# Performance work log

Hardware: AMD Instinct MI355X
Metric: run time of the kernel (lower is better)

The kernel has to match this reference:

```python
import jax, jax.numpy as jnp
import numpy as np

N_EMBD = 1024
N_HEAD = 16
B, L = 4, 2048


def setup_inputs() -> dict:
    key = jax.random.key(0)
    ks = jax.random.split(key, 5)
    scale = 1.0 / np.sqrt(N_EMBD)
    x = jax.random.normal(ks[0], (B, L, N_EMBD), dtype=jnp.float32)
    # nn.Linear(n_embd, n_embd, bias=False) weights, stored torch-style (out, in)
    Wq = jax.random.uniform(ks[1], (N_EMBD, N_EMBD), jnp.float32, -scale, scale)
    Wk = jax.random.uniform(ks[2], (N_EMBD, N_EMBD), jnp.float32, -scale, scale)
    Wv = jax.random.uniform(ks[3], (N_EMBD, N_EMBD), jnp.float32, -scale, scale)
    Wp = jax.random.uniform(ks[4], (N_EMBD, N_EMBD), jnp.float32, -scale, scale)
    attn_mask = jnp.ones((B, L), dtype=jnp.int32)
    return {"x": x, "Wq": Wq, "Wk": Wk, "Wv": Wv, "Wp": Wp, "attn_mask": attn_mask}


def reference(x, Wq, Wk, Wv, Wp, attn_mask):
    Bq, Lq, C = x.shape
    hd = C // N_HEAD
    # torch Linear: y = x @ W.T
    def split_heads(y):
        return y.reshape(Bq, Lq, N_HEAD, hd).transpose(0, 2, 1, 3)  # (B,H,L,hd)
    q = split_heads(x @ Wq.T)
    k = split_heads(x @ Wk.T)
    v = split_heads(x @ Wv.T)
    att = jnp.einsum("bhqd,bhkd->bhqk", q, k) / np.sqrt(hd)  # (B,H,L,L)
    causal = jnp.tril(jnp.ones((Lq, Lq), dtype=bool))
    neg_inf = jnp.float32(-jnp.inf)
    att = jnp.where(causal[None, None, :, :], att, neg_inf)
    pad = (attn_mask != 0)[:, None, None, :]  # (B,1,1,L) key-side padding mask
    att = jnp.where(pad, att, neg_inf)
    att = jax.nn.softmax(att, axis=-1)
    y = jnp.einsum("bhqk,bhkd->bhqd", att, v)
    y = y.transpose(0, 2, 1, 3).reshape(Bq, Lq, C)
    return y @ Wp.T
```

## Files before the change

### kernel.cpp

```cpp
#include <hip/hip_runtime.h>

typedef __attribute__((ext_vector_type(8))) short short8;
typedef __attribute__((ext_vector_type(4))) float floatx4;

#define CEMB 1024
#define NHEAD 16
#define HD 64
#define BATCH 4
#define SEQ 2048

#define BARRIER() asm volatile("s_waitcnt lgkmcnt(0)\n\ts_barrier" ::: "memory")

__device__ __forceinline__ unsigned short f2bf(float f) {
    union { float f; unsigned int i; } x; x.f = f;
    unsigned int r = x.i + 0x7FFFu + ((x.i >> 16) & 1u);
    return (unsigned short)(r >> 16);
}
__device__ __forceinline__ unsigned int packbf_trunc(float a, float b) {
    union { float f; unsigned int u; } x, y; x.f = a; y.f = b;
    return (x.u >> 16) | (y.u & 0xFFFF0000u);
}

#define GLD16(gp, lp) \
    __builtin_amdgcn_global_load_lds((const __attribute__((address_space(1))) void*)(gp), \
                                     (__attribute__((address_space(3))) void*)(lp), 16, 0, 0)

__global__ void cast_x(const float* __restrict__ src, unsigned short* __restrict__ dst, int n4) {
    int i = blockIdx.x * blockDim.x + threadIdx.x;
    if (i < n4) {
        float4 v = ((const float4*)src)[i];
        ushort4 o;
        o.x = f2bf(v.x); o.y = f2bf(v.y); o.z = f2bf(v.z); o.w = f2bf(v.w);
        ((ushort4*)dst)[i] = o;
    }
}

__global__ void cast_w(const float* __restrict__ w0, const float* __restrict__ w1,
                       const float* __restrict__ w2, const float* __restrict__ w3,
                       unsigned short* __restrict__ o0, unsigned short* __restrict__ o1,
                       unsigned short* __restrict__ o2, unsigned short* __restrict__ o3) {
    int which = blockIdx.y;
    const float* src = which == 0 ? w0 : which == 1 ? w1 : which == 2 ? w2 : w3;
    unsigned short* dst = which == 0 ? o0 : which == 1 ? o1 : which == 2 ? o2 : o3;
    float scale = (which == 0) ? 0.125f * 1.44269504088896f : 1.0f;
    int i = blockIdx.x * blockDim.x + threadIdx.x;
    float4 v = ((const float4*)src)[i];
    ushort4 o;
    o.x = f2bf(v.x * scale); o.y = f2bf(v.y * scale);
    o.z = f2bf(v.z * scale); o.w = f2bf(v.w * scale);
    ((ushort4*)dst)[i] = o;
}


#define MFMA __builtin_amdgcn_mfma_f32_16x16x32_bf16

#define PH(Ab, Bb, mh, nh) do {                                                 \
    short8 af[4][2], bfr[2][2];                                                 \
    _Pragma("unroll")                                                           \
    for (int mm = 0; mm < 4; ++mm) {                                            \
        af[mm][0] = *(const short8*)((Ab) + aOffR + (mh)*4096 + mm*1024 + ck0); \
        af[mm][1] = *(const short8*)((Ab) + aOffR + (mh)*4096 + mm*1024 + ck1); \
    }                                                                           \
    _Pragma("unroll")                                                           \
    for (int nn = 0; nn < 2; ++nn) {                                            \
        bfr[nn][0] = *(const short8*)((Bb) + bOffR + (nh)*2048 + nn*1024 + ck0);\
        bfr[nn][1] = *(const short8*)((Bb) + bOffR + (nh)*2048 + nn*1024 + ck1);\
    }                                                                           \
    __builtin_amdgcn_s_setprio(1);                                              \
    _Pragma("unroll")                                                           \
    for (int mm = 0; mm < 4; ++mm)                                              \
        _Pragma("unroll")                                                       \
        for (int nn = 0; nn < 2; ++nn) {                                        \
            acc[(mh)*4+mm][(nh)*2+nn] = MFMA(af[mm][0], bfr[nn][0],             \
                                             acc[(mh)*4+mm][(nh)*2+nn], 0,0,0); \
            acc[(mh)*4+mm][(nh)*2+nn] = MFMA(af[mm][1], bfr[nn][1],             \
                                             acc[(mh)*4+mm][(nh)*2+nn], 0,0,0); \
        }                                                                       \
    __builtin_amdgcn_s_setprio(0);                                              \
    __builtin_amdgcn_sched_barrier(0);                                          \
} while (0)

#define STAGE(Ab, Bb, k0) do {                                                  \
    GLD16(aS + (k0),             (Ab) + aLA);                                   \
    GLD16(aS + (k0) +  8 * CEMB, (Ab) + aLA + 512);                             \
    if constexpr (MH == 2) {                                                    \
        GLD16(aS + (k0) + 16 * CEMB, (Ab) + aLA + 1024);                        \
        GLD16(aS + (k0) + 24 * CEMB, (Ab) + aLA + 1536);                        \
    }                                                                           \
    GLD16(bS + (k0),             (Bb) + aLB);                                   \
    GLD16(bS + (k0) +  8 * CEMB, (Bb) + aLB + 512);                             \
    GLD16(bS + (k0) + 16 * CEMB, (Bb) + aLB + 1024);                            \
    GLD16(bS + (k0) + 24 * CEMB, (Bb) + aLB + 1536);                            \
} while (0)

#define PH4(Ab, Bb, MHL, t, do_stage) do {                                      \
    short8 af[4][2], bfr[2][2];                                                 \
    _Pragma("unroll")                                                           \
    for (int mm = 0; mm < 4; ++mm) {                                            \
        af[mm][0] = *(const short8*)((Ab) + aOffR + (MHL)*4096 + mm*1024 + ck0);\
        af[mm][1] = *(const short8*)((Ab) + aOffR + (MHL)*4096 + mm*1024 + ck1);\
    }                                                                           \
    _Pragma("unroll")                                                           \
    for (int nn = 0; nn < 2; ++nn) {                                            \
        bfr[nn][0] = *(const short8*)((Bb) + bOffR + 2048 + nn*1024 + ck0);     \
        bfr[nn][1] = *(const short8*)((Bb) + bOffR + 2048 + nn*1024 + ck1);     \
    }                                                                           \
    asm volatile("s_waitcnt lgkmcnt(0)\n\ts_barrier" ::: "memory");             \
    __builtin_amdgcn_sched_barrier(0);                                          \
    if (do_stage) STAGE(Ab, Bb, ((t) + 2) * 64);                                \
    __builtin_amdgcn_s_setprio(1);                                              \
    _Pragma("unroll")                                                           \
    for (int mm = 0; mm < 4; ++mm)                                              \
        _Pragma("unroll")                                                       \
        for (int nn = 0; nn < 2; ++nn) {                                        \
            acc[(MHL)*4+mm][2+nn] = MFMA(af[mm][0], bfr[nn][0],                 \
                                         acc[(MHL)*4+mm][2+nn], 0,0,0);         \
            acc[(MHL)*4+mm][2+nn] = MFMA(af[mm][1], bfr[nn][1],                 \
                                         acc[(MHL)*4+mm][2+nn], 0,0,0);         \
        }                                                                       \
    __builtin_amdgcn_s_setprio(0);                                              \
    __builtin_amdgcn_sched_barrier(0);                                          \
} while (0)

#define TILE(t, drain, do_stage) do {                                           \
    unsigned short* Ab = &As[(t) & 1][0];                                       \
    unsigned short* Bb = &Bs[(t) & 1][0];                                       \
    if (drain) { asm volatile("s_waitcnt vmcnt(0)" ::: "memory"); }             \
    else if constexpr (MH == 2) { asm volatile("s_waitcnt vmcnt(8)" ::: "memory"); } \
    else { asm volatile("s_waitcnt vmcnt(6)" ::: "memory"); }                   \
    asm volatile("s_barrier" ::: "memory");                                     \
    if constexpr (MH == 2) {                                                    \
        PH(Ab, Bb, 0, 0); PH(Ab, Bb, 1, 0); PH(Ab, Bb, 0, 1);                   \
        PH4(Ab, Bb, 1, t, do_stage);                                            \
    } else {                                                                    \
        PH(Ab, Bb, 0, 0);                                                       \
        PH4(Ab, Bb, 0, t, do_stage);                                            \
    }                                                                           \
} while (0)

template<int MH>
__launch_bounds__(512, 2)
__global__ void gemm_t(const unsigned short* __restrict__ A,
                       const unsigned short* __restrict__ W,
                       void* __restrict__ O0, void* __restrict__ O1,
                       void* __restrict__ O2, int mode, int ntn) {
    __shared__ unsigned short As[2][MH * 8192];
    __shared__ unsigned short Bs[2][16384];

    int nwg = gridDim.x;
    int bid = blockIdx.x;
    int wg = (bid & 7) * (nwg >> 3) + (bid >> 3);
    int mt = wg / ntn;
    int nt = wg - mt * ntn;
    int m0 = mt * (MH * 128), n0 = nt * 256;

    int tid = threadIdx.x;
    int wave = tid >> 6, lane = tid & 63;
    int l16 = lane & 15, quad = lane >> 4;
    int wm = wave >> 2, wn = wave & 3;

    int srow = lane >> 3;
    int scol = ((lane & 7) ^ srow) * 8;
    const unsigned short* aS = A + (size_t)(m0 + wave * (MH * 16) + srow) * CEMB + scol;
    const unsigned short* bS = W + (size_t)(n0 + wave * 32 + srow) * CEMB + scol;
    int aLA = wave * (MH * 1024);
    int aLB = wave * 2048;

    int aOffR = (wm * (MH * 64) + l16) * 64;
    int bOffR = (wn * 64 + l16) * 64;
    int ck0 = (quad ^ (l16 & 7)) * 8;
    int ck1 = ck0 ^ 32;

    floatx4 acc[MH * 4][4];
    #pragma unroll
    for (int mm = 0; mm < MH * 4; ++mm)
        #pragma unroll
        for (int nn = 0; nn < 4; ++nn) acc[mm][nn] = (floatx4){0.f, 0.f, 0.f, 0.f};

    STAGE(&As[0][0], &Bs[0][0], 0);
    STAGE(&As[1][0], &Bs[1][0], 64);

    #pragma unroll 2
    for (int t = 0; t < 14; ++t) { TILE(t, false, true); }
    TILE(14, false, false);
    TILE(15, true, false);

    if (mode == 1) {
        float* Of = (float*)O0;
        #pragma unroll
        for (int mf = 0; mf < MH * 4; ++mf)
            #pragma unroll
            for (int j = 0; j < 4; ++j) {
                int m = m0 + wm * (MH * 64) + mf * 16 + quad * 4 + j;
                #pragma unroll
                for (int nf = 0; nf < 4; ++nf) {
                    int n = n0 + wn * 64 + nf * 16 + l16;
                    Of[(size_t)m * CEMB + n] = acc[mf][nf][j];
                }
            }
    } else {
        int which = n0 >> 10;
        unsigned short* out = (unsigned short*)(which == 0 ? O0 : which == 1 ? O1 : O2);
        if (which < 2) {
            #pragma unroll
            for (int mf = 0; mf < MH * 4; ++mf)
                #pragma unroll
                for (int j = 0; j < 4; ++j) {
                    int m = m0 + wm * (MH * 64) + mf * 16 + quad * 4 + j;
                    int bb = m >> 11, ll = m & (SEQ - 1);
                    #pragma unroll
                    for (int nf = 0; nf < 4; ++nf) {
                        int n = (n0 & (CEMB - 1)) + wn * 64 + nf * 16 + l16;
                        int h = n >> 6, d = n & (HD - 1);
                        out[(size_t)((bb * NHEAD + h) * SEQ + ll) * HD + d] =
                            f2bf(acc[mf][nf][j]);
                    }
                }
        } else {
            #pragma unroll
            for (int mf = 0; mf < MH * 4; ++mf) {
                int m = m0 + wm * (MH * 64) + mf * 16 + quad * 4;
                int bb = m >> 11, ll = m & (SEQ - 1);
                #pragma unroll
                for (int nf = 0; nf < 4; ++nf) {
                    int n = (n0 & (CEMB - 1)) + wn * 64 + nf * 16 + l16;
                    int h = n >> 6, d = n & (HD - 1);
                    ushort4 o4;
                    o4.x = f2bf(acc[mf][nf][0]); o4.y = f2bf(acc[mf][nf][1]);
                    o4.z = f2bf(acc[mf][nf][2]); o4.w = f2bf(acc[mf][nf][3]);
                    *(ushort4*)&out[(size_t)((bb * NHEAD + h) * HD + d) * SEQ + ll] = o4;
                }
            }
        }
    }
}

__launch_bounds__(256, 2)
__global__ void attn_mfma(const unsigned short* __restrict__ Qb,
                          const unsigned short* __restrict__ Kb,
                          const unsigned short* __restrict__ Vtg,
                          const int* __restrict__ amask,
                          unsigned short* __restrict__ Yb) {
    __shared__ unsigned short Ks[64 * 64];
    __shared__ unsigned short Vs[64 * 64];
    __shared__ unsigned short Ps[128 * 64];

    int tid = threadIdx.x;
    int wave = tid >> 6;
    int lane = tid & 63;
    int l16 = lane & 15;
    int quad = lane >> 4;
    int l7 = l16 & 7;
    int pair = blockIdx.x;
    int bh = blockIdx.y;
    int bidx = bh >> 4;
    int h = bh & (NHEAD - 1);
    size_t hbase = (size_t)bh * SEQ * HD;

    int r0 = tid >> 3, p0 = tid & 7;
    int cl = p0 ^ (r0 & 7);
    unsigned short* kDst0 = Ks + r0 * 64 + p0 * 8;
    unsigned short* kDst1 = kDst0 + 32 * 64;
    unsigned short* vDst0 = Vs + r0 * 64 + p0 * 8;
    unsigned short* vDst1 = vDst0 + 32 * 64;
    const unsigned short* kSrc0 = Kb + hbase + (size_t)r0 * HD + cl * 8;
    const unsigned short* kSrc1 = kSrc0 + (size_t)32 * HD;
    const unsigned short* vSrc0 = Vtg + hbase + (size_t)r0 * SEQ + cl * 8;
    const unsigned short* vSrc1 = vSrc0 + (size_t)32 * SEQ;
    const int* mSrc = amask + bidx * SEQ + quad * 4;

    #pragma unroll
    for (int pass = 0; pass < 2; ++pass) {
        int qt = pass == 0 ? (15 - pair) : pair;
        int q0 = qt * 128;
        int nkt = 2 * qt + 2;

        short8 qf[2][2];
        #pragma unroll
        for (int qsub = 0; qsub < 2; ++qsub)
            #pragma unroll
            for (int kk = 0; kk < 2; ++kk)
                qf[qsub][kk] = *(const short8*)(Qb + hbase +
                    (size_t)(q0 + wave * 32 + qsub * 16 + l16) * HD + kk * 32 + quad * 8);

        short8 kr0 = *(const short8*)(kSrc0);
        short8 kr1 = *(const short8*)(kSrc1);
        short8 vr0 = *(const short8*)(vSrc0);
        short8 vr1 = *(const short8*)(vSrc1);
        int4 cmi[4];
        #pragma unroll
        for (int t = 0; t < 4; ++t) cmi[t] = *(const int4*)(mSrc + t * 16);

        floatx4 o[2][4];
        #pragma unroll
        for (int qsub = 0; qsub < 2; ++qsub)
            #pragma unroll
            for (int t = 0; t < 4; ++t) o[qsub][t] = (floatx4){0.f, 0.f, 0.f, 0.f};
        float ls[2] = {0.f, 0.f};

        int qw = q0 + wave * 32;

        for (int jt = 0; jt < nkt; ++jt) {
            BARRIER();
            *(short8*)kDst0 = kr0;
            *(short8*)kDst1 = kr1;
            *(short8*)vDst0 = vr0;
            *(short8*)vDst1 = vr1;
            int4 cm[4];
            #pragma unroll
            for (int t = 0; t < 4; ++t) cm[t] = cmi[t];
            if (jt + 1 < nkt) {
                size_t ko = (size_t)(jt + 1) * 64;
                kr0 = *(const short8*)(kSrc0 + ko * HD);
                kr1 = *(const short8*)(kSrc1 + ko * HD);
                vr0 = *(const short8*)(vSrc0 + ko);
                vr1 = *(const short8*)(vSrc1 + ko);
                #pragma unroll
                for (int t = 0; t < 4; ++t) cmi[t] = *(const int4*)(mSrc + (jt + 1) * 64 + t * 16);
            }
            BARRIER();

            if (jt * 64 <= qw + 31) {
                floatx4 sc[2][4];
                #pragma unroll
                for (int qsub = 0; qsub < 2; ++qsub)
                    #pragma unroll
                    for (int t = 0; t < 4; ++t) sc[qsub][t] = (floatx4){0.f, 0.f, 0.f, 0.f};
                #pragma unroll
                for (int kk = 0; kk < 2; ++kk)
                    #pragma unroll
                    for (int t = 0; t < 4; ++t) {
                        short8 aK = *(const short8*)(Ks + (t * 16 + l16) * 64 +
                                                     ((kk * 4 + quad) ^ l7) * 8);
                        #pragma unroll
                        for (int qsub = 0; qsub < 2; ++qsub)
                            sc[qsub][t] = __builtin_amdgcn_mfma_f32_16x16x32_bf16(
                                aK, qf[qsub][kk], sc[qsub][t], 0, 0, 0);
                    }

                bool needc = (jt * 64 + 63 > qw);

                #pragma unroll
                for (int qsub = 0; qsub < 2; ++qsub) {
                    int qi = q0 + wave * 32 + qsub * 16 + l16;
                    #pragma unroll
                    for (int t = 0; t < 4; ++t) {
                        int kb = jt * 64 + t * 16 + quad * 4;
                        float p[4];
                        #pragma unroll
                        for (int j = 0; j < 4; ++j) {
                            float sv = sc[qsub][t][j];
                            if (needc) sv = (kb + j <= qi) ? sv : -1e30f;
                            sv = cm[t][j] ? sv : -1e30f;
                            p[j] = exp2f(sv);
                            ls[qsub] += p[j];
                        }
                        int row = wave * 32 + qsub * 16 + l16;
                        int pos = (t * 2 + (quad >> 1)) ^ l7;
                        uint2 pk;
                        pk.x = packbf_trunc(p[0], p[1]);
                        pk.y = packbf_trunc(p[2], p[3]);
                        *(uint2*)(Ps + row * 64 + pos * 8 + (quad & 1) * 4) = pk;
                    }
                }

                #pragma unroll
                for (int kk = 0; kk < 2; ++kk) {
                    short8 pa[2];
                    #pragma unroll
                    for (int qsub = 0; qsub < 2; ++qsub)
                        pa[qsub] = *(const short8*)(Ps + (wave * 32 + qsub * 16 + l16) * 64 +
                                                    ((kk * 4 + quad) ^ l7) * 8);
                    #pragma unroll
                    for (int t = 0; t < 4; ++t) {
                        short8 vb = *(const short8*)(Vs + (t * 16 + l16) * 64 +
                                                     ((kk * 4 + quad) ^ l7) * 8);
                        #pragma unroll
                        for (int qsub = 0; qsub < 2; ++qsub)
                            o[qsub][t] = __builtin_amdgcn_mfma_f32_16x16x32_bf16(
                                pa[qsub], vb, o[qsub][t], 0, 0, 0);
                    }
                }
            }
        }

        #pragma unroll
        for (int qsub = 0; qsub < 2; ++qsub) {
            ls[qsub] += __shfl_xor(ls[qsub], 16, 64);
            ls[qsub] += __shfl_xor(ls[qsub], 32, 64);
        }

        #pragma unroll
        for (int qsub = 0; qsub < 2; ++qsub)
            #pragma unroll
            for (int j = 0; j < 4; ++j) {
                float lq = __shfl(ls[qsub], quad * 4 + j, 64);
                float inv = 1.0f / lq;
                size_t row = (size_t)bidx * SEQ + q0 + wave * 32 + qsub * 16 + quad * 4 + j;
                #pragma unroll
                for (int t = 0; t < 4; ++t)
                    Yb[row * CEMB + h * HD + t * 16 + l16] = f2bf(o[qsub][t][j] * inv);
            }
    }
}

extern "C" void kernel_launch(void* const* d_in, const int* in_sizes, int n_in,
                              void* d_out, int out_size, void* d_ws, size_t ws_size,
                              hipStream_t stream) {
    const float* x  = (const float*)d_in[0];
    const float* Wq = (const float*)d_in[1];
    const float* Wk = (const float*)d_in[2];
    const float* Wv = (const float*)d_in[3];
    const float* Wp = (const float*)d_in[4];
    const int* amask = (const int*)d_in[5];

    char* ws = (char*)d_ws;
    unsigned short* xb  = (unsigned short*)(ws + 0);
    unsigned short* Wqb = (unsigned short*)(ws + (16u << 20));
    unsigned short* Wkb = (unsigned short*)(ws + (18u << 20));
    unsigned short* Wvb = (unsigned short*)(ws + (20u << 20));
    unsigned short* Wpb = (unsigned short*)(ws + (22u << 20));
    unsigned short* Qb  = (unsigned short*)(ws + (24u << 20));
    unsigned short* Kb  = (unsigned short*)(ws + (40u << 20));
    unsigned short* Vtg = (unsigned short*)(ws + (56u << 20));
    unsigned short* Yb  = (unsigned short*)(ws + (72u << 20));

    const int NX4 = (BATCH * SEQ * CEMB) / 4;
    const int NW4 = (CEMB * CEMB) / 4;
    cast_x<<<dim3(NX4 / 256), 256, 0, stream>>>(x, xb, NX4);
    cast_w<<<dim3(NW4 / 256, 4), 256, 0, stream>>>(Wq, Wk, Wv, Wp, Wqb, Wkb, Wvb, Wpb);

    gemm_t<2><<<dim3(384), 512, 0, stream>>>(
        xb, Wqb, (void*)Qb, (void*)Kb, (void*)Vtg, 0, 12);

    attn_mfma<<<dim3(8, BATCH * NHEAD), 256, 0, stream>>>(Qb, Kb, Vtg, amask, Yb);

    gemm_t<1><<<dim3(256), 512, 0, stream>>>(
        Yb, Wpb, d_out, nullptr, nullptr, 1, 4);
}
```

Baseline: 279.5 us.

## Use 128-row GEMM tiles with grouped mapping and split attention into per-tile blocks

The QKV projection drops the 256-row templated tile and uses 128-row tiles, doubling the grid to 768 blocks, with a grouped block-to-tile mapping meant to improve L2 reuse. The attention kernel no longer pairs a short and a long query tile in one block. It launches one block per (batch-head, query tile), 1024 in total, with a permuted tile order to balance the causal workload, and uses the hardware exp2 intrinsic. This aims to raise occupancy and balance load across CUs, at the cost of more per-block overhead and less data reuse per block.

```diff
diff --git a/kernel.cpp b/kernel.cpp
--- a/kernel.cpp
+++ b/kernel.cpp
@@ -83,22 +83,18 @@
 #define STAGE(Ab, Bb, k0) do {                                                  \
     GLD16(aS + (k0),             (Ab) + aLA);                                   \
     GLD16(aS + (k0) +  8 * CEMB, (Ab) + aLA + 512);                             \
-    if constexpr (MH == 2) {                                                    \
-        GLD16(aS + (k0) + 16 * CEMB, (Ab) + aLA + 1024);                        \
-        GLD16(aS + (k0) + 24 * CEMB, (Ab) + aLA + 1536);                        \
-    }                                                                           \
     GLD16(bS + (k0),             (Bb) + aLB);                                   \
     GLD16(bS + (k0) +  8 * CEMB, (Bb) + aLB + 512);                             \
     GLD16(bS + (k0) + 16 * CEMB, (Bb) + aLB + 1024);                            \
     GLD16(bS + (k0) + 24 * CEMB, (Bb) + aLB + 1536);                            \
 } while (0)
 
-#define PH4(Ab, Bb, MHL, t, do_stage) do {                                      \
+#define PH4(Ab, Bb, t, do_stage) do {                                           \
     short8 af[4][2], bfr[2][2];                                                 \
     _Pragma("unroll")                                                           \
     for (int mm = 0; mm < 4; ++mm) {                                            \
-        af[mm][0] = *(const short8*)((Ab) + aOffR + (MHL)*4096 + mm*1024 + ck0);\
-        af[mm][1] = *(const short8*)((Ab) + aOffR + (MHL)*4096 + mm*1024 + ck1);\
+        af[mm][0] = *(const short8*)((Ab) + aOffR + mm*1024 + ck0);             \
+        af[mm][1] = *(const short8*)((Ab) + aOffR + mm*1024 + ck1);             \
     }                                                                           \
     _Pragma("unroll")                                                           \
     for (int nn = 0; nn < 2; ++nn) {                                            \
@@ -113,10 +109,8 @@
     for (int mm = 0; mm < 4; ++mm)                                              \
         _Pragma("unroll")                                                       \
         for (int nn = 0; nn < 2; ++nn) {                                        \
-            acc[(MHL)*4+mm][2+nn] = MFMA(af[mm][0], bfr[nn][0],                 \
-                                         acc[(MHL)*4+mm][2+nn], 0,0,0);         \
-            acc[(MHL)*4+mm][2+nn] = MFMA(af[mm][1], bfr[nn][1],                 \
-                                         acc[(MHL)*4+mm][2+nn], 0,0,0);         \
+            acc[mm][2+nn] = MFMA(af[mm][0], bfr[nn][0], acc[mm][2+nn], 0,0,0);  \
+            acc[mm][2+nn] = MFMA(af[mm][1], bfr[nn][1], acc[mm][2+nn], 0,0,0);  \
         }                                                                       \
     __builtin_amdgcn_s_setprio(0);                                              \
     __builtin_amdgcn_sched_barrier(0);                                          \
@@ -126,33 +120,29 @@
     unsigned short* Ab = &As[(t) & 1][0];                                       \
     unsigned short* Bb = &Bs[(t) & 1][0];                                       \
     if (drain) { asm volatile("s_waitcnt vmcnt(0)" ::: "memory"); }             \
-    else if constexpr (MH == 2) { asm volatile("s_waitcnt vmcnt(8)" ::: "memory"); } \
-    else { asm volatile("s_waitcnt vmcnt(6)" ::: "memory"); }                   \
+    else       { asm volatile("s_waitcnt vmcnt(6)" ::: "memory"); }             \
     asm volatile("s_barrier" ::: "memory");                                     \
-    if constexpr (MH == 2) {                                                    \
-        PH(Ab, Bb, 0, 0); PH(Ab, Bb, 1, 0); PH(Ab, Bb, 0, 1);                   \
-        PH4(Ab, Bb, 1, t, do_stage);                                            \
-    } else {                                                                    \
-        PH(Ab, Bb, 0, 0);                                                       \
-        PH4(Ab, Bb, 0, t, do_stage);                                            \
-    }                                                                           \
+    PH(Ab, Bb, 0, 0);                                                           \
+    PH4(Ab, Bb, t, do_stage);                                                   \
 } while (0)
 
-template<int MH>
 __launch_bounds__(512, 2)
-__global__ void gemm_t(const unsigned short* __restrict__ A,
-                       const unsigned short* __restrict__ W,
-                       void* __restrict__ O0, void* __restrict__ O1,
-                       void* __restrict__ O2, int mode, int ntn) {
-    __shared__ unsigned short As[2][MH * 8192];
+__global__ void gemm_128(const unsigned short* __restrict__ A,
+                         const unsigned short* __restrict__ W,
+                         void* __restrict__ O0, void* __restrict__ O1,
+                         void* __restrict__ O2, int mode, int ntn) {
+    __shared__ unsigned short As[2][8192];
     __shared__ unsigned short Bs[2][16384];
 
     int nwg = gridDim.x;
     int bid = blockIdx.x;
     int wg = (bid & 7) * (nwg >> 3) + (bid >> 3);
-    int mt = wg / ntn;
-    int nt = wg - mt * ntn;
-    int m0 = mt * (MH * 128), n0 = nt * 256;
+    int cpr = ntn >> 2;
+    int c = wg >> 5, r = wg & 31;
+    int cm = c / cpr, cn = c - cm * cpr;
+    int mt = cm * 8 + (r >> 2);
+    int nt = cn * 4 + (r & 3);
+    int m0 = mt * 128, n0 = nt * 256;
 
     int tid = threadIdx.x;
     int wave = tid >> 6, lane = tid & 63;
@@ -161,19 +151,19 @@
 
     int srow = lane >> 3;
     int scol = ((lane & 7) ^ srow) * 8;
-    const unsigned short* aS = A + (size_t)(m0 + wave * (MH * 16) + srow) * CEMB + scol;
+    const unsigned short* aS = A + (size_t)(m0 + wave * 16 + srow) * CEMB + scol;
     const unsigned short* bS = W + (size_t)(n0 + wave * 32 + srow) * CEMB + scol;
-    int aLA = wave * (MH * 1024);
+    int aLA = wave * 1024;
     int aLB = wave * 2048;
 
-    int aOffR = (wm * (MH * 64) + l16) * 64;
+    int aOffR = (wm * 64 + l16) * 64;
     int bOffR = (wn * 64 + l16) * 64;
     int ck0 = (quad ^ (l16 & 7)) * 8;
     int ck1 = ck0 ^ 32;
 
-    floatx4 acc[MH * 4][4];
-    #pragma unroll
-    for (int mm = 0; mm < MH * 4; ++mm)
+    floatx4 acc[4][4];
+    #pragma unroll
+    for (int mm = 0; mm < 4; ++mm)
         #pragma unroll
         for (int nn = 0; nn < 4; ++nn) acc[mm][nn] = (floatx4){0.f, 0.f, 0.f, 0.f};
 
@@ -188,10 +178,10 @@
     if (mode == 1) {
         float* Of = (float*)O0;
         #pragma unroll
-        for (int mf = 0; mf < MH * 4; ++mf)
+        for (int mf = 0; mf < 4; ++mf)
             #pragma unroll
             for (int j = 0; j < 4; ++j) {
-                int m = m0 + wm * (MH * 64) + mf * 16 + quad * 4 + j;
+                int m = m0 + wm * 64 + mf * 16 + quad * 4 + j;
                 #pragma unroll
                 for (int nf = 0; nf < 4; ++nf) {
                     int n = n0 + wn * 64 + nf * 16 + l16;
@@ -203,10 +193,10 @@
         unsigned short* out = (unsigned short*)(which == 0 ? O0 : which == 1 ? O1 : O2);
         if (which < 2) {
             #pragma unroll
-            for (int mf = 0; mf < MH * 4; ++mf)
+            for (int mf = 0; mf < 4; ++mf)
                 #pragma unroll
                 for (int j = 0; j < 4; ++j) {
-                    int m = m0 + wm * (MH * 64) + mf * 16 + quad * 4 + j;
+                    int m = m0 + wm * 64 + mf * 16 + quad * 4 + j;
                     int bb = m >> 11, ll = m & (SEQ - 1);
                     #pragma unroll
                     for (int nf = 0; nf < 4; ++nf) {
@@ -218,8 +208,8 @@
                 }
         } else {
             #pragma unroll
-            for (int mf = 0; mf < MH * 4; ++mf) {
-                int m = m0 + wm * (MH * 64) + mf * 16 + quad * 4;
+            for (int mf = 0; mf < 4; ++mf) {
+                int m = m0 + wm * 64 + mf * 16 + quad * 4;
                 int bb = m >> 11, ll = m & (SEQ - 1);
                 #pragma unroll
                 for (int nf = 0; nf < 4; ++nf) {
@@ -251,8 +241,17 @@
     int l16 = lane & 15;
     int quad = lane >> 4;
     int l7 = l16 & 7;
-    int pair = blockIdx.x;
-    int bh = blockIdx.y;
+
+    int n = blockIdx.x;
+    int rr = n >> 8;
+    int i = n & 255;
+    int base = i & 15;
+    int bh = (i >> 4) + (rr << 4);
+    int qt = (rr == 0) ? base
+           : (rr == 1) ? 15 - base
+           : (rr == 2) ? (base ^ 8)
+                       : 15 - (base ^ 8);
+
     int bidx = bh >> 4;
     int h = bh & (NHEAD - 1);
     size_t hbase = (size_t)bh * SEQ * HD;
@@ -269,139 +268,135 @@
     const unsigned short* vSrc1 = vSrc0 + (size_t)32 * SEQ;
     const int* mSrc = amask + bidx * SEQ + quad * 4;
 
-    #pragma unroll
-    for (int pass = 0; pass < 2; ++pass) {
-        int qt = pass == 0 ? (15 - pair) : pair;
-        int q0 = qt * 128;
-        int nkt = 2 * qt + 2;
-
-        short8 qf[2][2];
-        #pragma unroll
-        for (int qsub = 0; qsub < 2; ++qsub)
+    int q0 = qt * 128;
+    int nkt = 2 * qt + 2;
+
+    short8 qf[2][2];
+    #pragma unroll
+    for (int qsub = 0; qsub < 2; ++qsub)
+        #pragma unroll
+        for (int kk = 0; kk < 2; ++kk)
+            qf[qsub][kk] = *(const short8*)(Qb + hbase +
+                (size_t)(q0 + wave * 32 + qsub * 16 + l16) * HD + kk * 32 + quad * 8);
+
+    short8 kr0 = *(const short8*)(kSrc0);
+    short8 kr1 = *(const short8*)(kSrc1);
+    short8 vr0 = *(const short8*)(vSrc0);
+    short8 vr1 = *(const short8*)(vSrc1);
+    int4 cmi[4];
+    #pragma unroll
+    for (int t = 0; t < 4; ++t) cmi[t] = *(const int4*)(mSrc + t * 16);
+
+    floatx4 o[2][4];
+    #pragma unroll
+    for (int qsub = 0; qsub < 2; ++qsub)
+        #pragma unroll
+        for (int t = 0; t < 4; ++t) o[qsub][t] = (floatx4){0.f, 0.f, 0.f, 0.f};
+    float ls[2] = {0.f, 0.f};
+
+    int qw = q0 + wave * 32;
+
+    for (int jt = 0; jt < nkt; ++jt) {
+        BARRIER();
+        *(short8*)kDst0 = kr0;
+        *(short8*)kDst1 = kr1;
+        *(short8*)vDst0 = vr0;
+        *(short8*)vDst1 = vr1;
+        int4 cm[4];
+        #pragma unroll
+        for (int t = 0; t < 4; ++t) cm[t] = cmi[t];
+        if (jt + 1 < nkt) {
+            size_t ko = (size_t)(jt + 1) * 64;
+            kr0 = *(const short8*)(kSrc0 + ko * HD);
+            kr1 = *(const short8*)(kSrc1 + ko * HD);
+            vr0 = *(const short8*)(vSrc0 + ko);
+            vr1 = *(const short8*)(vSrc1 + ko);
+            #pragma unroll
+            for (int t = 0; t < 4; ++t) cmi[t] = *(const int4*)(mSrc + (jt + 1) * 64 + t * 16);
+        }
+        BARRIER();
+
+        if (jt * 64 <= qw + 31) {
+            floatx4 sc[2][4];
+            #pragma unroll
+            for (int qsub = 0; qsub < 2; ++qsub)
+                #pragma unroll
+                for (int t = 0; t < 4; ++t) sc[qsub][t] = (floatx4){0.f, 0.f, 0.f, 0.f};
             #pragma unroll
             for (int kk = 0; kk < 2; ++kk)
-                qf[qsub][kk] = *(const short8*)(Qb + hbase +
-                    (size_t)(q0 + wave * 32 + qsub * 16 + l16) * HD + kk * 32 + quad * 8);
-
-        short8 kr0 = *(const short8*)(kSrc0);
-        short8 kr1 = *(const short8*)(kSrc1);
-        short8 vr0 = *(const short8*)(vSrc0);
-        short8 vr1 = *(const short8*)(vSrc1);
-        int4 cmi[4];
-        #pragma unroll
-        for (int t = 0; t < 4; ++t) cmi[t] = *(const int4*)(mSrc + t * 16);
-
-        floatx4 o[2][4];
-        #pragma unroll
-        for (int qsub = 0; qsub < 2; ++qsub)
-            #pragma unroll
-            for (int t = 0; t < 4; ++t) o[qsub][t] = (floatx4){0.f, 0.f, 0.f, 0.f};
-        float ls[2] = {0.f, 0.f};
-
-        int qw = q0 + wave * 32;
-
-        for (int jt = 0; jt < nkt; ++jt) {
-            BARRIER();
-            *(short8*)kDst0 = kr0;
-            *(short8*)kDst1 = kr1;
-            *(short8*)vDst0 = vr0;
-            *(short8*)vDst1 = vr1;
-            int4 cm[4];
-            #pragma unroll
-            for (int t = 0; t < 4; ++t) cm[t] = cmi[t];
-            if (jt + 1 < nkt) {
-                size_t ko = (size_t)(jt + 1) * 64;
-                kr0 = *(const short8*)(kSrc0 + ko * HD);
-                kr1 = *(const short8*)(kSrc1 + ko * HD);
-                vr0 = *(const short8*)(vSrc0 + ko);
-                vr1 = *(const short8*)(vSrc1 + ko);
-                #pragma unroll
-                for (int t = 0; t < 4; ++t) cmi[t] = *(const int4*)(mSrc + (jt + 1) * 64 + t * 16);
-            }
-            BARRIER();
-
-            if (jt * 64 <= qw + 31) {
-                floatx4 sc[2][4];
-                #pragma unroll
-                for (int qsub = 0; qsub < 2; ++qsub)
-                    #pragma unroll
-                    for (int t = 0; t < 4; ++t) sc[qsub][t] = (floatx4){0.f, 0.f, 0.f, 0.f};
-                #pragma unroll
-                for (int kk = 0; kk < 2; ++kk)
-                    #pragma unroll
-                    for (int t = 0; t < 4; ++t) {
-                        short8 aK = *(const short8*)(Ks + (t * 16 + l16) * 64 +
-                                                     ((kk * 4 + quad) ^ l7) * 8);
-                        #pragma unroll
-                        for (int qsub = 0; qsub < 2; ++qsub)
-                            sc[qsub][t] = __builtin_amdgcn_mfma_f32_16x16x32_bf16(
-                                aK, qf[qsub][kk], sc[qsub][t], 0, 0, 0);
-                    }
-
-                bool needc = (jt * 64 + 63 > qw);
-
-                #pragma unroll
-                for (int qsub = 0; qsub < 2; ++qsub) {
-                    int qi = q0 + wave * 32 + qsub * 16 + l16;
-                    #pragma unroll
-                    for (int t = 0; t < 4; ++t) {
-                        int kb = jt * 64 + t * 16 + quad * 4;
-                        float p[4];
-                        #pragma unroll
-                        for (int j = 0; j < 4; ++j) {
-                            float sv = sc[qsub][t][j];
-                            if (needc) sv = (kb + j <= qi) ? sv : -1e30f;
-                            sv = cm[t][j] ? sv : -1e30f;
-                            p[j] = exp2f(sv);
-                            ls[qsub] += p[j];
-                        }
-                        int row = wave * 32 + qsub * 16 + l16;
-                        int pos = (t * 2 + (quad >> 1)) ^ l7;
-                        uint2 pk;
-                        pk.x = packbf_trunc(p[0], p[1]);
-                        pk.y = packbf_trunc(p[2], p[3]);
-                        *(uint2*)(Ps + row * 64 + pos * 8 + (quad & 1) * 4) = pk;
-                    }
-                }
-
-                #pragma unroll
-                for (int kk = 0; kk < 2; ++kk) {
-                    short8 pa[2];
+                #pragma unroll
+                for (int t = 0; t < 4; ++t) {
+                    short8 aK = *(const short8*)(Ks + (t * 16 + l16) * 64 +
+                                                 ((kk * 4 + quad) ^ l7) * 8);
                     #pragma unroll
                     for (int qsub = 0; qsub < 2; ++qsub)
-                        pa[qsub] = *(const short8*)(Ps + (wave * 32 + qsub * 16 + l16) * 64 +
-                                                    ((kk * 4 + quad) ^ l7) * 8);
+                        sc[qsub][t] = __builtin_amdgcn_mfma_f32_16x16x32_bf16(
+                            aK, qf[qsub][kk], sc[qsub][t], 0, 0, 0);
+                }
+
+            bool needc = (jt * 64 + 63 > qw);
+
+            #pragma unroll
+            for (int qsub = 0; qsub < 2; ++qsub) {
+                int qi = q0 + wave * 32 + qsub * 16 + l16;
+                #pragma unroll
+                for (int t = 0; t < 4; ++t) {
+                    int kb = jt * 64 + t * 16 + quad * 4;
+                    float p[4];
                     #pragma unroll
-                    for (int t = 0; t < 4; ++t) {
-                        short8 vb = *(const short8*)(Vs + (t * 16 + l16) * 64 +
-                                                     ((kk * 4 + quad) ^ l7) * 8);
-                        #pragma unroll
-                        for (int qsub = 0; qsub < 2; ++qsub)
-                            o[qsub][t] = __builtin_amdgcn_mfma_f32_16x16x32_bf16(
-                                pa[qsub], vb, o[qsub][t], 0, 0, 0);
+                    for (int j = 0; j < 4; ++j) {
+                        float sv = sc[qsub][t][j];
+                        if (needc) sv = (kb + j <= qi) ? sv : -1e30f;
+                        sv = cm[t][j] ? sv : -1e30f;
+                        p[j] = __builtin_amdgcn_exp2f(sv);
+                        ls[qsub] += p[j];
                     }
+                    int row = wave * 32 + qsub * 16 + l16;
+                    int pos = (t * 2 + (quad >> 1)) ^ l7;
+                    uint2 pk;
+                    pk.x = packbf_trunc(p[0], p[1]);
+                    pk.y = packbf_trunc(p[2], p[3]);
+                    *(uint2*)(Ps + row * 64 + pos * 8 + (quad & 1) * 4) = pk;
+                }
+            }
+
+            #pragma unroll
+            for (int kk = 0; kk < 2; ++kk) {
+                short8 pa[2];
+                #pragma unroll
+                for (int qsub = 0; qsub < 2; ++qsub)
+                    pa[qsub] = *(const short8*)(Ps + (wave * 32 + qsub * 16 + l16) * 64 +
+                                                ((kk * 4 + quad) ^ l7) * 8);
+                #pragma unroll
+                for (int t = 0; t < 4; ++t) {
+                    short8 vb = *(const short8*)(Vs + (t * 16 + l16) * 64 +
+                                                 ((kk * 4 + quad) ^ l7) * 8);
+                    #pragma unroll
+                    for (int qsub = 0; qsub < 2; ++qsub)
+                        o[qsub][t] = __builtin_amdgcn_mfma_f32_16x16x32_bf16(
+                            pa[qsub], vb, o[qsub][t], 0, 0, 0);
                 }
             }
         }
-
-        #pragma unroll
-        for (int qsub = 0; qsub < 2; ++qsub) {
-            ls[qsub] += __shfl_xor(ls[qsub], 16, 64);
-            ls[qsub] += __shfl_xor(ls[qsub], 32, 64);
+    }
+
+    #pragma unroll
+    for (int qsub = 0; qsub < 2; ++qsub) {
+        ls[qsub] += __shfl_xor(ls[qsub], 16, 64);
+        ls[qsub] += __shfl_xor(ls[qsub], 32, 64);
+    }
+
+    #pragma unroll
+    for (int qsub = 0; qsub < 2; ++qsub)
+        #pragma unroll
+        for (int j = 0; j < 4; ++j) {
+            float lq = __shfl(ls[qsub], quad * 4 + j, 64);
+            float inv = 1.0f / lq;
+            size_t row = (size_t)bidx * SEQ + q0 + wave * 32 + qsub * 16 + quad * 4 + j;
+            #pragma unroll
+            for (int t = 0; t < 4; ++t)
+                Yb[row * CEMB + h * HD + t * 16 + l16] = f2bf(o[qsub][t][j] * inv);
         }
-
-        #pragma unroll
-        for (int qsub = 0; qsub < 2; ++qsub)
-            #pragma unroll
-            for (int j = 0; j < 4; ++j) {
-                float lq = __shfl(ls[qsub], quad * 4 + j, 64);
-                float inv = 1.0f / lq;
-                size_t row = (size_t)bidx * SEQ + q0 + wave * 32 + qsub * 16 + quad * 4 + j;
-                #pragma unroll
-                for (int t = 0; t < 4; ++t)
-                    Yb[row * CEMB + h * HD + t * 16 + l16] = f2bf(o[qsub][t][j] * inv);
-            }
-    }
 }
 
 extern "C" void kernel_launch(void* const* d_in, const int* in_sizes, int n_in,
@@ -430,11 +425,11 @@
     cast_x<<<dim3(NX4 / 256), 256, 0, stream>>>(x, xb, NX4);
     cast_w<<<dim3(NW4 / 256, 4), 256, 0, stream>>>(Wq, Wk, Wv, Wp, Wqb, Wkb, Wvb, Wpb);
 
-    gemm_t<2><<<dim3(384), 512, 0, stream>>>(
+    gemm_128<<<dim3(768), 512, 0, stream>>>(
         xb, Wqb, (void*)Qb, (void*)Kb, (void*)Vtg, 0, 12);
 
-    attn_mfma<<<dim3(8, BATCH * NHEAD), 256, 0, stream>>>(Qb, Kb, Vtg, amask, Yb);
-
-    gemm_t<1><<<dim3(256), 512, 0, stream>>>(
+    attn_mfma<<<dim3(1024), 256, 0, stream>>>(Qb, Kb, Vtg, amask, Yb);
+
+    gemm_128<<<dim3(256), 512, 0, stream>>>(
         Yb, Wpb, d_out, nullptr, nullptr, 1, 4);
 }
```

Measured after the change: 256.0 us. -8.4%, faster.
